# Kernel tuning notes

Measured on AMD Instinct MI355X. Metric: run time of the kernel, lower is better.

The kernel has to match this reference:

```python
import jax, jax.numpy as jnp
import numpy as np

H = 8      # num_heads
D = 768    # hidden_dim
DH = D // H
L = 2      # num_attention_layers
B = 64     # graph pairs in batch
N = 4096   # nodes per side
EPS = 1e-5


def setup_inputs() -> dict:
    key = jax.random.key(0)
    ks = jax.random.split(key, 16)
    h1 = jax.random.normal(ks[0], (N, D), dtype=jnp.float32)
    h2 = jax.random.normal(ks[1], (N, D), dtype=jnp.float32)
    # same key for both batch vectors -> identical sorted ids, every pair id
    # present on both sides (realistic paired graphs, no empty attention rows)
    batch = jnp.sort(jax.random.randint(ks[2], (N,), 0, B)).astype(jnp.int64)
    batch1 = batch
    batch2 = batch
    s = 0.02
    Wq = jax.random.normal(ks[3], (L, D, D), jnp.float32) * s
    Wk = jax.random.normal(ks[4], (L, D, D), jnp.float32) * s
    Wv = jax.random.normal(ks[5], (L, D, D), jnp.float32) * s
    Wo = jax.random.normal(ks[6], (L, D, D), jnp.float32) * s
    bq = jnp.zeros((L, D), jnp.float32)
    bk = jnp.zeros((L, D), jnp.float32)
    bv = jnp.zeros((L, D), jnp.float32)
    bo = jnp.zeros((L, D), jnp.float32)
    ln_g = jnp.ones((2 * L, D), jnp.float32)
    ln_b = jnp.zeros((2 * L, D), jnp.float32)
    mW1 = jax.random.normal(ks[7], (2 * D, D), jnp.float32) * s
    mb1 = jnp.zeros((D,), jnp.float32)
    mW2 = jax.random.normal(ks[8], (D, 1), jnp.float32) * s
    mb2 = jnp.zeros((1,), jnp.float32)
    return {"h1": h1, "h2": h2, "batch1": batch1, "batch2": batch2,
            "Wq": Wq, "bq": bq, "Wk": Wk, "bk": bk, "Wv": Wv, "bv": bv,
            "Wo": Wo, "bo": bo, "ln_g": ln_g, "ln_b": ln_b,
            "mW1": mW1, "mb1": mb1, "mW2": mW2, "mb2": mb2}


def _layer_norm(x, g, b):
    mu = jnp.mean(x, axis=-1, keepdims=True)
    var = jnp.var(x, axis=-1, keepdims=True)
    return (x - mu) * jax.lax.rsqrt(var + EPS) * g + b


def _cross_attn(xq, xkv, mask, Wq, bq, Wk, bk, Wv, bv, Wo, bo):
    # multi-head cross attention, queries from xq, keys/values from xkv
    nq = xq.shape[0]
    q = (xq @ Wq + bq).reshape(nq, H, DH)
    k = (xkv @ Wk + bk).reshape(-1, H, DH)
    v = (xkv @ Wv + bv).reshape(-1, H, DH)
    scores = jnp.einsum('nhd,mhd->hnm', q, k) / jnp.sqrt(jnp.asarray(DH, xq.dtype))
    scores = jnp.where(mask[None, :, :], scores, jnp.asarray(-1e9, xq.dtype))
    attn = jax.nn.softmax(scores, axis=-1)  # [H, Nq, Nkv]
    out = jnp.einsum('hnm,mhd->nhd', attn, v).reshape(nq, D)
    return out @ Wo + bo


def _aggregate(x, batch):
    # mean_max aggregation: scatter_mean + scatter_max over graph ids
    ssum = jax.ops.segment_sum(x, batch, num_segments=B)
    cnt = jax.ops.segment_sum(jnp.ones((x.shape[0],), x.dtype), batch, num_segments=B)
    mean = ssum / jnp.maximum(cnt, 1.0)[:, None]
    smax = jax.ops.segment_max(x, batch, num_segments=B)
    smax = jnp.where(cnt[:, None] > 0, smax, 0.0)
    return mean + smax


def reference(h1, h2, batch1, batch2, Wq, bq, Wk, bk, Wv, bv, Wo, bo,
              ln_g, ln_b, mW1, mb1, mW2, mb2):
    batch1 = batch1.astype(jnp.int32)
    batch2 = batch2.astype(jnp.int32)
    mask_12 = batch1[:, None] == batch2[None, :]  # [N1, N2]
    mask_21 = mask_12.T
    h1_out, h2_out = h1, h2
    for i in range(L):
        m12 = _cross_attn(h1_out, h2_out, mask_12,
                          Wq[i], bq[i], Wk[i], bk[i], Wv[i], bv[i], Wo[i], bo[i])
        h1_out = _layer_norm(h1_out + m12, ln_g[2 * i], ln_b[2 * i])
        m21 = _cross_attn(h2_out, h1_out, mask_21,
                          Wq[i], bq[i], Wk[i], bk[i], Wv[i], bv[i], Wo[i], bo[i])
        h2_out = _layer_norm(h2_out + m21, ln_g[2 * i + 1], ln_b[2 * i + 1])
    g1 = _aggregate(h1_out, batch1)
    g2 = _aggregate(h2_out, batch2)
    combined = jnp.concatenate([g1, g2], axis=-1)  # [B, 2D]
    hid = jax.nn.relu(combined @ mW1 + mb1)
    return jax.nn.sigmoid(hid @ mW2 + mb2)  # [B, 1]
```

## Files before the change

### kernel.cpp

```cpp
#include <hip/hip_runtime.h>
#include <hip/hip_bf16.h>

#define N_NODES 4096
#define DIM 768
#define NH 8
#define DH 96
#define NB 64
#define NL 2

typedef unsigned short ushort_t;
typedef __attribute__((ext_vector_type(8))) short bf16x8;
typedef __attribute__((ext_vector_type(4))) float f32x4;

typedef __attribute__((address_space(1))) const unsigned int gas_uint;
typedef __attribute__((address_space(3))) unsigned int las_uint;

__device__ inline float bf2f(unsigned int u16) {
    union { unsigned int i; float f; } v;
    v.i = u16 << 16;
    return v.f;
}
__device__ inline ushort_t f2bf(float f) {
    union { float f; unsigned int i; } v;
    v.f = f;
    unsigned int u = v.i;
    return (ushort_t)((u + 0x7fffu + ((u >> 16) & 1u)) >> 16);
}

__device__ inline void gld16(const ushort_t* g, const ushort_t* l) {
    __builtin_amdgcn_global_load_lds((gas_uint*)g, (las_uint*)l, 16, 0, 0);
}

__global__ __launch_bounds__(128) void seg_kernel(const int* __restrict__ b1,
                                                  const int* __restrict__ b2,
                                                  int* __restrict__ seg) {
    int t = threadIdx.x;
    const int* arr = (t < 64) ? b1 : b2;
    int b = t & 63;
    int base = (t < 64) ? 0 : 128;
    int lo = 0, hi = N_NODES;
    while (lo < hi) { int mid = (lo + hi) >> 1; if (arr[mid] < b) lo = mid + 1; else hi = mid; }
    int s = lo;
    hi = N_NODES;
    while (lo < hi) { int mid = (lo + hi) >> 1; if (arr[mid] < b + 1) lo = mid + 1; else hi = mid; }
    seg[base + b] = s;
    seg[base + 64 + b] = lo;
}

__global__ __launch_bounds__(256) void cast_in2(const float* __restrict__ s1,
                                                const float* __restrict__ s2,
                                                float* __restrict__ d1,
                                                float* __restrict__ d2,
                                                ushort_t* __restrict__ db1,
                                                ushort_t* __restrict__ db2) {
    int side = blockIdx.y;
    const float* src = side ? s2 : s1;
    float* dst = side ? d2 : d1;
    ushort_t* dstb = side ? db2 : db1;
    int i = blockIdx.x * 256 + threadIdx.x;
    float4 v = ((const float4*)src)[i];
    ((float4*)dst)[i] = v;
    uint2 p;
    p.x = (unsigned)f2bf(v.x) | ((unsigned)f2bf(v.y) << 16);
    p.y = (unsigned)f2bf(v.z) | ((unsigned)f2bf(v.w) << 16);
    ((uint2*)dstb)[i] = p;
}

__global__ __launch_bounds__(256) void wtcast_all(const float* __restrict__ Wq,
                                                  const float* __restrict__ Wk,
                                                  const float* __restrict__ Wv,
                                                  const float* __restrict__ Wo,
                                                  ushort_t* __restrict__ Wbt) {
    __shared__ float t[32][33];
    int z = blockIdx.z;
    int which = z >> 1, l = z & 1;
    const float* W = (which == 0) ? Wq : (which == 1) ? Wk : (which == 2) ? Wv : Wo;
    W += (size_t)l * DIM * DIM;
    ushort_t* Wt = Wbt + (size_t)(which * NL + l) * DIM * DIM;
    int tx = threadIdx.x & 31, ty = threadIdx.x >> 5;
    int k0 = blockIdx.x * 32, n0 = blockIdx.y * 32;
#pragma unroll
    for (int i = 0; i < 4; ++i)
        t[ty + 8 * i][tx] = W[(size_t)(k0 + ty + 8 * i) * DIM + n0 + tx];
    __syncthreads();
#pragma unroll
    for (int i = 0; i < 4; ++i)
        Wt[(size_t)(n0 + ty + 8 * i) * DIM + k0 + tx] = f2bf(t[tx][ty + 8 * i]);
}

__global__ __launch_bounds__(256) void w1cast(const float* __restrict__ W1,
                                              ushort_t* __restrict__ W1b) {
    int i = blockIdx.x * 256 + threadIdx.x;
    float4 v = ((const float4*)W1)[i];
    uint2 p;
    p.x = (unsigned)f2bf(v.x) | ((unsigned)f2bf(v.y) << 16);
    p.y = (unsigned)f2bf(v.z) | ((unsigned)f2bf(v.w) << 16);
    ((uint2*)W1b)[i] = p;
}

template <int BM, int OUT_BF16>
__device__ inline void gemm_body(const ushort_t* __restrict__ X,
                                 const ushort_t* __restrict__ W,
                                 const float* __restrict__ bias,
                                 ushort_t* __restrict__ outB,
                                 float* __restrict__ outF,
                                 int brow, int bcol) {
    __shared__ alignas(16) ushort_t As[BM * 32];
    __shared__ alignas(16) ushort_t Bs[128 * 32];
    constexpr int NJ = (BM == 128) ? 4 : 2;
    int tid = threadIdx.x;
    int lane = tid & 63, wid = tid >> 6;
    int WR = (BM == 128) ? (wid >> 1) : 0;
    int WC = (BM == 128) ? (wid & 1) : wid;

    f32x4 acc[4][NJ];
#pragma unroll
    for (int m = 0; m < 4; ++m)
#pragma unroll
        for (int n = 0; n < NJ; ++n)
            acc[m][n] = (f32x4){0.f, 0.f, 0.f, 0.f};

    int srow = lane >> 2;
    int sslot = (lane & 3) ^ ((lane >> 3) & 3);
    int aRow0 = (BM == 128) ? (wid * 32) : (wid * 16);
    const ushort_t* aS = X + (size_t)(brow + aRow0 + srow) * DIM + sslot * 8;
    const ushort_t* bS = W + (size_t)(bcol + wid * 32 + srow) * DIM + sslot * 8;
    const ushort_t* ldsA = As + aRow0 * 32;
    const ushort_t* ldsB = Bs + wid * 32 * 32;

    int fr = lane & 15;
    int fslot = (lane >> 4) ^ ((lane >> 1) & 3);
    const char* Ab = (const char*)As;
    const char* Bb = (const char*)Bs;

    for (int kc = 0; kc < DIM; kc += 32) {
        __syncthreads();
        gld16(aS + kc, ldsA);
        if (BM == 128) gld16(aS + kc + (size_t)16 * DIM, ldsA + 16 * 32);
        gld16(bS + kc, ldsB);
        gld16(bS + kc + (size_t)16 * DIM, ldsB + 16 * 32);
        __syncthreads();
        bf16x8 af[4], bfr[NJ];
#pragma unroll
        for (int m = 0; m < 4; ++m)
            af[m] = *(const bf16x8*)(Ab + (size_t)(WR * 64 + m * 16 + fr) * 64 + fslot * 16);
#pragma unroll
        for (int n = 0; n < NJ; ++n)
            bfr[n] = *(const bf16x8*)(Bb + (size_t)(WC * (16 * NJ) + n * 16 + fr) * 64 + fslot * 16);
#pragma unroll
        for (int m = 0; m < 4; ++m)
#pragma unroll
            for (int n = 0; n < NJ; ++n)
                acc[m][n] = __builtin_amdgcn_mfma_f32_16x16x32_bf16(af[m], bfr[n], acc[m][n], 0, 0, 0);
    }

#pragma unroll
    for (int m = 0; m < 4; ++m)
#pragma unroll
        for (int n = 0; n < NJ; ++n) {
            int col = bcol + WC * (16 * NJ) + n * 16 + (lane & 15);
            float bv = bias[col];
#pragma unroll
            for (int j = 0; j < 4; ++j) {
                int row = brow + WR * 64 + m * 16 + (lane >> 4) * 4 + j;
                float v = acc[m][n][j] + bv;
                if (OUT_BF16) outB[(size_t)row * DIM + col] = f2bf(v);
                else outF[(size_t)row * DIM + col] = v;
            }
        }
}

struct QKVArgs {
    const ushort_t* Xq;
    const ushort_t* Xkv;
    const ushort_t* W0; const ushort_t* W1; const ushort_t* W2;
    const float* b0; const float* b1; const float* b2;
    ushort_t* O0; ushort_t* O1; ushort_t* O2;
};

__global__ __launch_bounds__(256) void qkv_gemm(QKVArgs a) {
    int z = blockIdx.z;
    const ushort_t* X = (z == 0) ? a.Xq : a.Xkv;
    const ushort_t* W = (z == 0) ? a.W0 : (z == 1) ? a.W1 : a.W2;
    const float* b = (z == 0) ? a.b0 : (z == 1) ? a.b1 : a.b2;
    ushort_t* O = (z == 0) ? a.O0 : (z == 1) ? a.O1 : a.O2;
    gemm_body<128, 1>(X, W, b, O, nullptr, blockIdx.x * 128, blockIdx.y * 128);
}

__global__ __launch_bounds__(256) void o_gemm(const ushort_t* __restrict__ X,
                                              const ushort_t* __restrict__ W,
                                              const float* __restrict__ b,
                                              float* __restrict__ Out) {
    gemm_body<64, 0>(X, W, b, nullptr, Out, blockIdx.x * 64, blockIdx.y * 128);
}

#define MAXSEG 192
#define NKP 200
__global__ __launch_bounds__(256) void attn_mfma(const ushort_t* __restrict__ Q,
                                                 const ushort_t* __restrict__ K,
                                                 const ushort_t* __restrict__ V,
                                                 ushort_t* __restrict__ M,
                                                 const int* __restrict__ seg,
                                                 int qbase, int kvbase) {
    __shared__ alignas(16) ushort_t VT[96 * NKP];
    __shared__ alignas(16) ushort_t PL[4 * 16 * NKP];
    int b = blockIdx.x, h = blockIdx.y;
    int tid = threadIdx.x, lane = tid & 63, wid = tid >> 6;
    int qs = seg[qbase + b], qe = seg[qbase + 64 + b];
    int ks = seg[kvbase + b], ke = seg[kvbase + 64 + b];
    int nq = qe - qs, nk = ke - ks;
    if (nq <= 0) return;
    if (nk > MAXSEG) nk = MAXSEG;
    if (nk <= 0) {
        for (int q = qs + wid; q < qe; q += 4)
            for (int c = lane; c < DH; c += 64)
                M[(size_t)q * DIM + h * DH + c] = 0;
        return;
    }
    int nkp32 = (nk + 31) & ~31;
    int nkt = nkp32 >> 4;
    int nk2 = nkp32 >> 5;

    for (int idx = tid; idx < nkp32 * 12; idx += 256) {
        int j = idx / 12, c = idx - j * 12;
        ushort_t tmp[8];
        if (j < nk) {
            *(uint4*)tmp = *(const uint4*)(V + (size_t)(ks + j) * DIM + h * DH + c * 8);
        } else {
#pragma unroll
            for (int r = 0; r < 8; ++r) tmp[r] = 0;
        }
#pragma unroll
        for (int r = 0; r < 8; ++r)
            VT[(size_t)(c * 8 + r) * NKP + j] = tmp[r];
    }
    __syncthreads();

    const float scale = 0.1020620726159658f;
    int fr = lane & 15;
    int koff = (lane >> 4) * 8;
    ushort_t* pl = PL + (size_t)wid * 16 * NKP;

    for (int qt = wid; qt * 16 < nq; qt += 4) {
        int qrow = qs + qt * 16 + fr;
        if (qrow > qe - 1) qrow = qe - 1;
        const ushort_t* qp = Q + (size_t)qrow * DIM + h * DH + koff;
        bf16x8 af0 = *(const bf16x8*)(qp);
        bf16x8 af1 = *(const bf16x8*)(qp + 32);
        bf16x8 af2 = *(const bf16x8*)(qp + 64);

        f32x4 sc[12];
#pragma unroll
        for (int kt = 0; kt < 12; ++kt) {
            if (kt >= nkt) continue;
            int key = ks + kt * 16 + fr;
            if (key > ke - 1) key = ke - 1;
            const ushort_t* kp = K + (size_t)key * DIM + h * DH + koff;
            f32x4 a = (f32x4){0.f, 0.f, 0.f, 0.f};
            a = __builtin_amdgcn_mfma_f32_16x16x32_bf16(af0, *(const bf16x8*)(kp), a, 0, 0, 0);
            a = __builtin_amdgcn_mfma_f32_16x16x32_bf16(af1, *(const bf16x8*)(kp + 32), a, 0, 0, 0);
            a = __builtin_amdgcn_mfma_f32_16x16x32_bf16(af2, *(const bf16x8*)(kp + 64), a, 0, 0, 0);
            sc[kt] = a;
        }

        float mrow[4] = {-1e30f, -1e30f, -1e30f, -1e30f};
#pragma unroll
        for (int kt = 0; kt < 12; ++kt) {
            if (kt >= nkt) continue;
            bool valid = (kt * 16 + fr) < nk;
#pragma unroll
            for (int j = 0; j < 4; ++j) {
                float s = valid ? sc[kt][j] * scale : -1e30f;
                sc[kt][j] = s;
                mrow[j] = fmaxf(mrow[j], s);
            }
        }
#pragma unroll
        for (int j = 0; j < 4; ++j) {
            mrow[j] = fmaxf(mrow[j], __shfl_xor(mrow[j], 1, 64));
            mrow[j] = fmaxf(mrow[j], __shfl_xor(mrow[j], 2, 64));
            mrow[j] = fmaxf(mrow[j], __shfl_xor(mrow[j], 4, 64));
            mrow[j] = fmaxf(mrow[j], __shfl_xor(mrow[j], 8, 64));
        }
        float rsum[4] = {0.f, 0.f, 0.f, 0.f};
#pragma unroll
        for (int kt = 0; kt < 12; ++kt) {
            if (kt >= nkt) continue;
#pragma unroll
            for (int j = 0; j < 4; ++j) {
                float p = __expf(sc[kt][j] - mrow[j]);
                sc[kt][j] = p;
                rsum[j] += p;
            }
        }
#pragma unroll
        for (int j = 0; j < 4; ++j) {
            rsum[j] += __shfl_xor(rsum[j], 1, 64);
            rsum[j] += __shfl_xor(rsum[j], 2, 64);
            rsum[j] += __shfl_xor(rsum[j], 4, 64);
            rsum[j] += __shfl_xor(rsum[j], 8, 64);
        }
        float rinv[4];
#pragma unroll
        for (int j = 0; j < 4; ++j) rinv[j] = 1.f / rsum[j];

#pragma unroll
        for (int kt = 0; kt < 12; ++kt) {
            if (kt >= nkt) continue;
#pragma unroll
            for (int j = 0; j < 4; ++j)
                pl[(size_t)((lane >> 4) * 4 + j) * NKP + kt * 16 + fr] = f2bf(sc[kt][j]);
        }

        f32x4 oacc[6];
#pragma unroll
        for (int nt = 0; nt < 6; ++nt) oacc[nt] = (f32x4){0.f, 0.f, 0.f, 0.f};
#pragma unroll
        for (int k2 = 0; k2 < 6; ++k2) {
            if (k2 >= nk2) continue;
            bf16x8 pa = *(const bf16x8*)(pl + (size_t)fr * NKP + k2 * 32 + koff);
#pragma unroll
            for (int nt = 0; nt < 6; ++nt) {
                bf16x8 vb = *(const bf16x8*)(VT + (size_t)(nt * 16 + fr) * NKP + k2 * 32 + koff);
                oacc[nt] = __builtin_amdgcn_mfma_f32_16x16x32_bf16(pa, vb, oacc[nt], 0, 0, 0);
            }
        }

#pragma unroll
        for (int nt = 0; nt < 6; ++nt)
#pragma unroll
            for (int j = 0; j < 4; ++j) {
                int qr = qt * 16 + (lane >> 4) * 4 + j;
                if (qr < nq)
                    M[(size_t)(qs + qr) * DIM + h * DH + nt * 16 + fr] = f2bf(oacc[nt][j] * rinv[j]);
            }
    }
}

__global__ __launch_bounds__(256) void add_ln_kernel(float* __restrict__ h,
                                                     ushort_t* __restrict__ hb,
                                                     const float* __restrict__ o,
                                                     const float* __restrict__ g,
                                                     const float* __restrict__ bb) {
    int row = blockIdx.x * 4 + (threadIdx.x >> 6);
    int lane = threadIdx.x & 63;
    float* hp = h + (size_t)row * DIM;
    const float* op = o + (size_t)row * DIM;
    float x[12];
    float s = 0.f, s2 = 0.f;
#pragma unroll
    for (int k = 0; k < 3; ++k) {
        int c = lane * 4 + k * 256;
        float4 a = *(const float4*)(hp + c);
        float4 bv = *(const float4*)(op + c);
        float v0 = a.x + bv.x, v1 = a.y + bv.y, v2 = a.z + bv.z, v3 = a.w + bv.w;
        x[4 * k + 0] = v0; x[4 * k + 1] = v1; x[4 * k + 2] = v2; x[4 * k + 3] = v3;
        s += (v0 + v1) + (v2 + v3);
        s2 += v0 * v0 + v1 * v1 + v2 * v2 + v3 * v3;
    }
#pragma unroll
    for (int off = 32; off; off >>= 1) {
        s += __shfl_xor(s, off, 64);
        s2 += __shfl_xor(s2, off, 64);
    }
    float mu = s * (1.f / 768.f);
    float var = s2 * (1.f / 768.f) - mu * mu;
    float rstd = rsqrtf(var + 1e-5f);
#pragma unroll
    for (int k = 0; k < 3; ++k) {
        int c = lane * 4 + k * 256;
        float4 gv = *(const float4*)(g + c);
        float4 bv = *(const float4*)(bb + c);
        float4 y;
        y.x = (x[4 * k + 0] - mu) * rstd * gv.x + bv.x;
        y.y = (x[4 * k + 1] - mu) * rstd * gv.y + bv.y;
        y.z = (x[4 * k + 2] - mu) * rstd * gv.z + bv.z;
        y.w = (x[4 * k + 3] - mu) * rstd * gv.w + bv.w;
        *(float4*)(hp + c) = y;
        uint2 p;
        p.x = (unsigned)f2bf(y.x) | ((unsigned)f2bf(y.y) << 16);
        p.y = (unsigned)f2bf(y.z) | ((unsigned)f2bf(y.w) << 16);
        *(uint2*)(hb + (size_t)row * DIM + c) = p;
    }
}

__global__ __launch_bounds__(256) void agg_kernel(const float* __restrict__ h1,
                                                  const float* __restrict__ h2,
                                                  const int* __restrict__ seg,
                                                  float* __restrict__ G) {
    int b = blockIdx.x, side = blockIdx.y;
    int c = blockIdx.z * 256 + threadIdx.x;
    const float* hp = side ? h2 : h1;
    int s = seg[side * 128 + b], e = seg[side * 128 + 64 + b];
    int cnt = e - s;
    float sum = 0.f, mx = -1e30f;
    int i = s;
    for (; i + 4 <= e; i += 4) {
        float v0 = hp[(size_t)(i + 0) * DIM + c];
        float v1 = hp[(size_t)(i + 1) * DIM + c];
        float v2 = hp[(size_t)(i + 2) * DIM + c];
        float v3 = hp[(size_t)(i + 3) * DIM + c];
        sum += v0 + v1 + v2 + v3;
        mx = fmaxf(fmaxf(mx, fmaxf(v0, v1)), fmaxf(v2, v3));
    }
    for (; i < e; ++i) {
        float v = hp[(size_t)i * DIM + c];
        sum += v;
        mx = fmaxf(mx, v);
    }
    G[(size_t)b * 1536 + side * DIM + c] = (cnt > 0) ? (sum / (float)cnt + mx) : 0.f;
}

__global__ __launch_bounds__(256) void mlp1_kernel(const float* __restrict__ G,
                                                   const ushort_t* __restrict__ W1b,
                                                   const float* __restrict__ b1,
                                                   float* __restrict__ Hid) {
    __shared__ float gs[4][1536];
    __shared__ float red[7][32][17];
    int bg = blockIdx.x;
    int jc = blockIdx.y;
    int tid = threadIdx.x;
    int jq = tid & 31;
    int kq = tid >> 5;
    int j = jc * 128 + jq * 4;

    for (int idx = tid; idx < 4 * 1536 / 4; idx += 256)
        ((float4*)&gs[0][0])[idx] = ((const float4*)(G + (size_t)bg * 4 * 1536))[idx];
    __syncthreads();

    float acc[4][4] = {};
    const ushort_t* wp = W1b + (size_t)(kq * 192) * DIM + j;
    for (int i = 0; i < 192; ++i) {
        uint2 w = *(const uint2*)(wp + (size_t)i * DIM);
        float w0 = bf2f(w.x & 0xffffu), w1 = bf2f(w.x >> 16);
        float w2 = bf2f(w.y & 0xffffu), w3 = bf2f(w.y >> 16);
        int krow = kq * 192 + i;
#pragma unroll
        for (int bb = 0; bb < 4; ++bb) {
            float gv = gs[bb][krow];
            acc[bb][0] += gv * w0; acc[bb][1] += gv * w1;
            acc[bb][2] += gv * w2; acc[bb][3] += gv * w3;
        }
    }
    if (kq) {
#pragma unroll
        for (int bb = 0; bb < 4; ++bb)
#pragma unroll
            for (int c = 0; c < 4; ++c)
                red[kq - 1][jq][bb * 4 + c] = acc[bb][c];
    }
    __syncthreads();
    if (kq == 0) {
        float4 bv = *(const float4*)(b1 + j);
#pragma unroll
        for (int bb = 0; bb < 4; ++bb) {
            float r[4];
#pragma unroll
            for (int c = 0; c < 4; ++c) {
                r[c] = acc[bb][c];
#pragma unroll
                for (int q = 0; q < 7; ++q) r[c] += red[q][jq][bb * 4 + c];
            }
            float4 o;
            o.x = fmaxf(r[0] + bv.x, 0.f);
            o.y = fmaxf(r[1] + bv.y, 0.f);
            o.z = fmaxf(r[2] + bv.z, 0.f);
            o.w = fmaxf(r[3] + bv.w, 0.f);
            *(float4*)(Hid + (size_t)(bg * 4 + bb) * DIM + j) = o;
        }
    }
}

__global__ __launch_bounds__(256) void mlp2_kernel(const float* __restrict__ Hid,
                                                   const float* __restrict__ W2,
                                                   const float* __restrict__ b2,
                                                   float* __restrict__ out) {
    int b = blockIdx.x, tid = threadIdx.x;
    float s = 0.f;
    for (int j = tid; j < DIM; j += 256) s += Hid[(size_t)b * DIM + j] * W2[j];
#pragma unroll
    for (int off = 32; off; off >>= 1) s += __shfl_xor(s, off, 64);
    __shared__ float rs[4];
    if ((tid & 63) == 0) rs[tid >> 6] = s;
    __syncthreads();
    if (tid == 0) {
        float t = rs[0] + rs[1] + rs[2] + rs[3] + b2[0];
        out[b] = 1.f / (1.f + expf(-t));
    }
}

extern "C" void kernel_launch(void* const* d_in, const int* in_sizes, int n_in,
                              void* d_out, int out_size, void* d_ws, size_t ws_size,
                              hipStream_t stream) {
    const float* h1 = (const float*)d_in[0];
    const float* h2 = (const float*)d_in[1];
    const int* batch1 = (const int*)d_in[2];
    const int* batch2 = (const int*)d_in[3];
    const float* Wq = (const float*)d_in[4];
    const float* bq = (const float*)d_in[5];
    const float* Wk = (const float*)d_in[6];
    const float* bk = (const float*)d_in[7];
    const float* Wv = (const float*)d_in[8];
    const float* bv = (const float*)d_in[9];
    const float* Wo = (const float*)d_in[10];
    const float* bo = (const float*)d_in[11];
    const float* ln_g = (const float*)d_in[12];
    const float* ln_b = (const float*)d_in[13];
    const float* mW1 = (const float*)d_in[14];
    const float* mb1 = (const float*)d_in[15];
    const float* mW2 = (const float*)d_in[16];
    const float* mb2 = (const float*)d_in[17];
    float* out = (float*)d_out;

    const size_t ND = (size_t)N_NODES * DIM;
    const size_t WSZ = (size_t)DIM * DIM;
    float* h1c = (float*)d_ws;
    float* h2c = h1c + ND;
    float* G = h2c + ND;
    float* Hid = G + 64 * 1536;
    ushort_t* h1b = (ushort_t*)(Hid + 64 * DIM);
    ushort_t* h2b = h1b + ND;
    ushort_t* Qb = h2b + ND;
    ushort_t* Kb = Qb + ND;
    ushort_t* Vb = Kb + ND;
    ushort_t* Mbb = Vb + ND;
    ushort_t* Wbt = Mbb + ND;
    ushort_t* W1bf = Wbt + 8 * WSZ;
    int* seg = (int*)(W1bf + (size_t)1536 * DIM);
    float* Ob = (float*)Qb;

    seg_kernel<<<1, 128, 0, stream>>>(batch1, batch2, seg);
    cast_in2<<<dim3((int)(ND / 4 / 256), 2), 256, 0, stream>>>(h1, h2, h1c, h2c, h1b, h2b);
    wtcast_all<<<dim3(24, 24, 8), 256, 0, stream>>>(Wq, Wk, Wv, Wo, Wbt);
    w1cast<<<(1536 * DIM / 4) / 256, 256, 0, stream>>>(mW1, W1bf);

    dim3 qkvg(32, 6, 3), og(64, 6), ag(64, 8);
    for (int i = 0; i < NL; ++i) {
        const ushort_t* wtq = Wbt + (0 * NL + i) * WSZ;
        const ushort_t* wtk = Wbt + (1 * NL + i) * WSZ;
        const ushort_t* wtv = Wbt + (2 * NL + i) * WSZ;
        const ushort_t* wto = Wbt + (3 * NL + i) * WSZ;
        const float* bqi = bq + (size_t)i * DIM;
        const float* bki = bk + (size_t)i * DIM;
        const float* bvi = bv + (size_t)i * DIM;
        const float* boi = bo + (size_t)i * DIM;

        QKVArgs a1 = {h1b, h2b, wtq, wtk, wtv, bqi, bki, bvi, Qb, Kb, Vb};
        qkv_gemm<<<qkvg, 256, 0, stream>>>(a1);
        attn_mfma<<<ag, 256, 0, stream>>>(Qb, Kb, Vb, Mbb, seg, 0, 128);
        o_gemm<<<og, 256, 0, stream>>>(Mbb, wto, boi, Ob);
        add_ln_kernel<<<N_NODES / 4, 256, 0, stream>>>(h1c, h1b, Ob,
                                                       ln_g + (size_t)(2 * i) * DIM,
                                                       ln_b + (size_t)(2 * i) * DIM);

        QKVArgs a2 = {h2b, h1b, wtq, wtk, wtv, bqi, bki, bvi, Qb, Kb, Vb};
        qkv_gemm<<<qkvg, 256, 0, stream>>>(a2);
        attn_mfma<<<ag, 256, 0, stream>>>(Qb, Kb, Vb, Mbb, seg, 128, 0);
        o_gemm<<<og, 256, 0, stream>>>(Mbb, wto, boi, Ob);
        add_ln_kernel<<<N_NODES / 4, 256, 0, stream>>>(h2c, h2b, Ob,
                                                       ln_g + (size_t)(2 * i + 1) * DIM,
                                                       ln_b + (size_t)(2 * i + 1) * DIM);
    }
    agg_kernel<<<dim3(64, 2, 3), 256, 0, stream>>>(h1c, h2c, seg, G);
    mlp1_kernel<<<dim3(16, 6), 256, 0, stream>>>(G, W1bf, mb1, Hid);
    mlp2_kernel<<<64, 256, 0, stream>>>(Hid, mW2, mb2, out);
}
```

Baseline: 337.9 us.

## Widen GEMM K-tile to 64, hoist Q2 projection into first QKV launch, merge prep kernels

The shared GEMM body now stages a 64-wide K chunk per barrier pair with a new XOR swizzle, which halves the number of sync rounds and global-to-LDS issue phases. The second half-layer's query projection depends only on h2, which is unchanged at that point, so it is computed in the first QKV launch (4 z-slices) into a new Q2 buffer. The second QKV launch then shrinks to a K/V-only GEMM. The seg, input-cast and W1-cast kernels are merged into one prep launch to cut launch count. LDS use per block doubles, which may lower occupancy.

```diff
diff --git a/kernel.cpp b/kernel.cpp
--- a/kernel.cpp
+++ b/kernel.cpp
@@ -31,39 +31,51 @@
     __builtin_amdgcn_global_load_lds((gas_uint*)g, (las_uint*)l, 16, 0, 0);
 }
 
-__global__ __launch_bounds__(128) void seg_kernel(const int* __restrict__ b1,
-                                                  const int* __restrict__ b2,
-                                                  int* __restrict__ seg) {
-    int t = threadIdx.x;
-    const int* arr = (t < 64) ? b1 : b2;
-    int b = t & 63;
-    int base = (t < 64) ? 0 : 128;
-    int lo = 0, hi = N_NODES;
-    while (lo < hi) { int mid = (lo + hi) >> 1; if (arr[mid] < b) lo = mid + 1; else hi = mid; }
-    int s = lo;
-    hi = N_NODES;
-    while (lo < hi) { int mid = (lo + hi) >> 1; if (arr[mid] < b + 1) lo = mid + 1; else hi = mid; }
-    seg[base + b] = s;
-    seg[base + 64 + b] = lo;
-}
-
-__global__ __launch_bounds__(256) void cast_in2(const float* __restrict__ s1,
-                                                const float* __restrict__ s2,
-                                                float* __restrict__ d1,
-                                                float* __restrict__ d2,
-                                                ushort_t* __restrict__ db1,
-                                                ushort_t* __restrict__ db2) {
-    int side = blockIdx.y;
-    const float* src = side ? s2 : s1;
-    float* dst = side ? d2 : d1;
-    ushort_t* dstb = side ? db2 : db1;
-    int i = blockIdx.x * 256 + threadIdx.x;
-    float4 v = ((const float4*)src)[i];
-    ((float4*)dst)[i] = v;
-    uint2 p;
-    p.x = (unsigned)f2bf(v.x) | ((unsigned)f2bf(v.y) << 16);
-    p.y = (unsigned)f2bf(v.z) | ((unsigned)f2bf(v.w) << 16);
-    ((uint2*)dstb)[i] = p;
+__global__ __launch_bounds__(256) void prep_kernel(const float* __restrict__ s1,
+                                                   const float* __restrict__ s2,
+                                                   float* __restrict__ d1,
+                                                   float* __restrict__ d2,
+                                                   ushort_t* __restrict__ db1,
+                                                   ushort_t* __restrict__ db2,
+                                                   const float* __restrict__ mW1,
+                                                   ushort_t* __restrict__ W1b,
+                                                   const int* __restrict__ bt1,
+                                                   const int* __restrict__ bt2,
+                                                   int* __restrict__ seg) {
+    int z = blockIdx.z;
+    int tid = threadIdx.x;
+    if (z < 2) {
+        const float* src = z ? s2 : s1;
+        float* dst = z ? d2 : d1;
+        ushort_t* dstb = z ? db2 : db1;
+        int i = blockIdx.x * 256 + tid;
+        float4 v = ((const float4*)src)[i];
+        ((float4*)dst)[i] = v;
+        uint2 p;
+        p.x = (unsigned)f2bf(v.x) | ((unsigned)f2bf(v.y) << 16);
+        p.y = (unsigned)f2bf(v.z) | ((unsigned)f2bf(v.w) << 16);
+        ((uint2*)dstb)[i] = p;
+        return;
+    }
+    if (blockIdx.x < 1152) {
+        int i = blockIdx.x * 256 + tid;
+        float4 v = ((const float4*)mW1)[i];
+        uint2 p;
+        p.x = (unsigned)f2bf(v.x) | ((unsigned)f2bf(v.y) << 16);
+        p.y = (unsigned)f2bf(v.z) | ((unsigned)f2bf(v.w) << 16);
+        ((uint2*)W1b)[i] = p;
+    } else if (blockIdx.x == 2000 && tid < 128) {
+        const int* arr = (tid < 64) ? bt1 : bt2;
+        int b = tid & 63;
+        int base = (tid < 64) ? 0 : 128;
+        int lo = 0, hi = N_NODES;
+        while (lo < hi) { int mid = (lo + hi) >> 1; if (arr[mid] < b) lo = mid + 1; else hi = mid; }
+        int s = lo;
+        hi = N_NODES;
+        while (lo < hi) { int mid = (lo + hi) >> 1; if (arr[mid] < b + 1) lo = mid + 1; else hi = mid; }
+        seg[base + b] = s;
+        seg[base + 64 + b] = lo;
+    }
 }
 
 __global__ __launch_bounds__(256) void wtcast_all(const float* __restrict__ Wq,
@@ -88,16 +100,6 @@
         Wt[(size_t)(n0 + ty + 8 * i) * DIM + k0 + tx] = f2bf(t[tx][ty + 8 * i]);
 }
 
-__global__ __launch_bounds__(256) void w1cast(const float* __restrict__ W1,
-                                              ushort_t* __restrict__ W1b) {
-    int i = blockIdx.x * 256 + threadIdx.x;
-    float4 v = ((const float4*)W1)[i];
-    uint2 p;
-    p.x = (unsigned)f2bf(v.x) | ((unsigned)f2bf(v.y) << 16);
-    p.y = (unsigned)f2bf(v.z) | ((unsigned)f2bf(v.w) << 16);
-    ((uint2*)W1b)[i] = p;
-}
-
 template <int BM, int OUT_BF16>
 __device__ inline void gemm_body(const ushort_t* __restrict__ X,
                                  const ushort_t* __restrict__ W,
@@ -105,9 +107,10 @@
                                  ushort_t* __restrict__ outB,
                                  float* __restrict__ outF,
                                  int brow, int bcol) {
-    __shared__ alignas(16) ushort_t As[BM * 32];
-    __shared__ alignas(16) ushort_t Bs[128 * 32];
+    __shared__ alignas(16) ushort_t As[BM * 64];
+    __shared__ alignas(16) ushort_t Bs[128 * 64];
     constexpr int NJ = (BM == 128) ? 4 : 2;
+    constexpr int AROWS = BM / 4;
     int tid = threadIdx.x;
     int lane = tid & 63, wid = tid >> 6;
     int WR = (BM == 128) ? (wid >> 1) : 0;
@@ -120,38 +123,44 @@
         for (int n = 0; n < NJ; ++n)
             acc[m][n] = (f32x4){0.f, 0.f, 0.f, 0.f};
 
-    int srow = lane >> 2;
-    int sslot = (lane & 3) ^ ((lane >> 3) & 3);
-    int aRow0 = (BM == 128) ? (wid * 32) : (wid * 16);
+    int srow = lane >> 3;
+    int sslot = (lane & 7) ^ srow;
+    int aRow0 = wid * AROWS;
     const ushort_t* aS = X + (size_t)(brow + aRow0 + srow) * DIM + sslot * 8;
     const ushort_t* bS = W + (size_t)(bcol + wid * 32 + srow) * DIM + sslot * 8;
-    const ushort_t* ldsA = As + aRow0 * 32;
-    const ushort_t* ldsB = Bs + wid * 32 * 32;
+    const ushort_t* ldsA = As + aRow0 * 64;
+    const ushort_t* ldsB = Bs + wid * 32 * 64;
 
     int fr = lane & 15;
-    int fslot = (lane >> 4) ^ ((lane >> 1) & 3);
+    int u = lane >> 4;
     const char* Ab = (const char*)As;
     const char* Bb = (const char*)Bs;
 
-    for (int kc = 0; kc < DIM; kc += 32) {
+    for (int kc = 0; kc < DIM; kc += 64) {
         __syncthreads();
-        gld16(aS + kc, ldsA);
-        if (BM == 128) gld16(aS + kc + (size_t)16 * DIM, ldsA + 16 * 32);
-        gld16(bS + kc, ldsB);
-        gld16(bS + kc + (size_t)16 * DIM, ldsB + 16 * 32);
+#pragma unroll
+        for (int t = 0; t < AROWS / 8; ++t)
+            gld16(aS + kc + (size_t)(8 * t) * DIM, ldsA + (8 * t) * 64);
+#pragma unroll
+        for (int t = 0; t < 4; ++t)
+            gld16(bS + kc + (size_t)(8 * t) * DIM, ldsB + (8 * t) * 64);
         __syncthreads();
-        bf16x8 af[4], bfr[NJ];
-#pragma unroll
-        for (int m = 0; m < 4; ++m)
-            af[m] = *(const bf16x8*)(Ab + (size_t)(WR * 64 + m * 16 + fr) * 64 + fslot * 16);
-#pragma unroll
-        for (int n = 0; n < NJ; ++n)
-            bfr[n] = *(const bf16x8*)(Bb + (size_t)(WC * (16 * NJ) + n * 16 + fr) * 64 + fslot * 16);
-#pragma unroll
-        for (int m = 0; m < 4; ++m)
+#pragma unroll
+        for (int kk = 0; kk < 2; ++kk) {
+            int slot = (kk * 4 + u) ^ (fr & 7);
+            bf16x8 af[4], bfr[NJ];
+#pragma unroll
+            for (int m = 0; m < 4; ++m)
+                af[m] = *(const bf16x8*)(Ab + (size_t)(WR * 64 + m * 16 + fr) * 128 + slot * 16);
 #pragma unroll
             for (int n = 0; n < NJ; ++n)
-                acc[m][n] = __builtin_amdgcn_mfma_f32_16x16x32_bf16(af[m], bfr[n], acc[m][n], 0, 0, 0);
+                bfr[n] = *(const bf16x8*)(Bb + (size_t)(WC * (16 * NJ) + n * 16 + fr) * 128 + slot * 16);
+#pragma unroll
+            for (int m = 0; m < 4; ++m)
+#pragma unroll
+                for (int n = 0; n < NJ; ++n)
+                    acc[m][n] = __builtin_amdgcn_mfma_f32_16x16x32_bf16(af[m], bfr[n], acc[m][n], 0, 0, 0);
+        }
     }
 
 #pragma unroll
@@ -170,21 +179,33 @@
         }
 }
 
-struct QKVArgs {
-    const ushort_t* Xq;
+struct QKV4Args {
+    const ushort_t* Xq1;
     const ushort_t* Xkv;
-    const ushort_t* W0; const ushort_t* W1; const ushort_t* W2;
-    const float* b0; const float* b1; const float* b2;
-    ushort_t* O0; ushort_t* O1; ushort_t* O2;
+    const ushort_t* Wq; const ushort_t* Wk; const ushort_t* Wv;
+    const float* bq; const float* bk; const float* bv;
+    ushort_t* Q1; ushort_t* K1; ushort_t* V1; ushort_t* Q2;
 };
 
-__global__ __launch_bounds__(256) void qkv_gemm(QKVArgs a) {
+__global__ __launch_bounds__(256) void qkv4_gemm(QKV4Args a) {
     int z = blockIdx.z;
-    const ushort_t* X = (z == 0) ? a.Xq : a.Xkv;
-    const ushort_t* W = (z == 0) ? a.W0 : (z == 1) ? a.W1 : a.W2;
-    const float* b = (z == 0) ? a.b0 : (z == 1) ? a.b1 : a.b2;
-    ushort_t* O = (z == 0) ? a.O0 : (z == 1) ? a.O1 : a.O2;
+    const ushort_t* X = (z == 0) ? a.Xq1 : a.Xkv;
+    const ushort_t* W = (z == 1) ? a.Wk : (z == 2) ? a.Wv : a.Wq;
+    const float* b = (z == 1) ? a.bk : (z == 2) ? a.bv : a.bq;
+    ushort_t* O = (z == 0) ? a.Q1 : (z == 1) ? a.K1 : (z == 2) ? a.V1 : a.Q2;
     gemm_body<128, 1>(X, W, b, O, nullptr, blockIdx.x * 128, blockIdx.y * 128);
+}
+
+__global__ __launch_bounds__(256) void kv_gemm(const ushort_t* __restrict__ X,
+                                               const ushort_t* __restrict__ Wk,
+                                               const ushort_t* __restrict__ Wv,
+                                               const float* __restrict__ bk,
+                                               const float* __restrict__ bv,
+                                               ushort_t* __restrict__ K,
+                                               ushort_t* __restrict__ V) {
+    int z = blockIdx.z;
+    gemm_body<128, 1>(X, z ? Wv : Wk, z ? bv : bk, z ? V : K, nullptr,
+                      blockIdx.x * 128, blockIdx.y * 128);
 }
 
 __global__ __launch_bounds__(256) void o_gemm(const ushort_t* __restrict__ X,
@@ -524,17 +545,17 @@
     ushort_t* Kb = Qb + ND;
     ushort_t* Vb = Kb + ND;
     ushort_t* Mbb = Vb + ND;
-    ushort_t* Wbt = Mbb + ND;
+    ushort_t* Q2b = Mbb + ND;
+    ushort_t* Wbt = Q2b + ND;
     ushort_t* W1bf = Wbt + 8 * WSZ;
     int* seg = (int*)(W1bf + (size_t)1536 * DIM);
     float* Ob = (float*)Qb;
 
-    seg_kernel<<<1, 128, 0, stream>>>(batch1, batch2, seg);
-    cast_in2<<<dim3((int)(ND / 4 / 256), 2), 256, 0, stream>>>(h1, h2, h1c, h2c, h1b, h2b);
+    prep_kernel<<<dim3(3072, 1, 3), 256, 0, stream>>>(h1, h2, h1c, h2c, h1b, h2b,
+                                                      mW1, W1bf, batch1, batch2, seg);
     wtcast_all<<<dim3(24, 24, 8), 256, 0, stream>>>(Wq, Wk, Wv, Wo, Wbt);
-    w1cast<<<(1536 * DIM / 4) / 256, 256, 0, stream>>>(mW1, W1bf);
-
-    dim3 qkvg(32, 6, 3), og(64, 6), ag(64, 8);
+
+    dim3 q4g(32, 6, 4), kvg(32, 6, 2), og(64, 6), ag(64, 8);
     for (int i = 0; i < NL; ++i) {
         const ushort_t* wtq = Wbt + (0 * NL + i) * WSZ;
         const ushort_t* wtk = Wbt + (1 * NL + i) * WSZ;
@@ -545,17 +566,16 @@
         const float* bvi = bv + (size_t)i * DIM;
         const float* boi = bo + (size_t)i * DIM;
 
-        QKVArgs a1 = {h1b, h2b, wtq, wtk, wtv, bqi, bki, bvi, Qb, Kb, Vb};
-        qkv_gemm<<<qkvg, 256, 0, stream>>>(a1);
+        QKV4Args a1 = {h1b, h2b, wtq, wtk, wtv, bqi, bki, bvi, Qb, Kb, Vb, Q2b};
+        qkv4_gemm<<<q4g, 256, 0, stream>>>(a1);
         attn_mfma<<<ag, 256, 0, stream>>>(Qb, Kb, Vb, Mbb, seg, 0, 128);
         o_gemm<<<og, 256, 0, stream>>>(Mbb, wto, boi, Ob);
         add_ln_kernel<<<N_NODES / 4, 256, 0, stream>>>(h1c, h1b, Ob,
                                                        ln_g + (size_t)(2 * i) * DIM,
                                                        ln_b + (size_t)(2 * i) * DIM);
 
-        QKVArgs a2 = {h2b, h1b, wtq, wtk, wtv, bqi, bki, bvi, Qb, Kb, Vb};
-        qkv_gemm<<<qkvg, 256, 0, stream>>>(a2);
-        attn_mfma<<<ag, 256, 0, stream>>>(Qb, Kb, Vb, Mbb, seg, 128, 0);
+        kv_gemm<<<kvg, 256, 0, stream>>>(h1b, wtk, wtv, bki, bvi, Kb, Vb);
+        attn_mfma<<<ag, 256, 0, stream>>>(Q2b, Kb, Vb, Mbb, seg, 128, 0);
         o_gemm<<<og, 256, 0, stream>>>(Mbb, wto, boi, Ob);
         add_ln_kernel<<<N_NODES / 4, 256, 0, stream>>>(h2c, h2b, Ob,
                                                        ln_g + (size_t)(2 * i + 1) * DIM,
```

Result: slower. 384.4 us (+13.7%).
